# Kernel tuning notes

Hardware: AMD Instinct MI355X
Metric: run time of the kernel (lower is better)

Reference implementation:

```python
import jax, jax.numpy as jnp
import numpy as np

B, L, C, H = 2, 2048, 1024, 16  # batches, tokens per batch, channels, heads


def _ln(x, eps=1e-6):
    # LayerNorm32: no affine, eps=1e-6, computed in fp32
    x32 = x.astype(jnp.float32)
    m = x32.mean(-1, keepdims=True)
    v = ((x32 - m) ** 2).mean(-1, keepdims=True)
    return ((x32 - m) * jax.lax.rsqrt(v + eps)).astype(x.dtype)


def setup_inputs() -> dict:
    key = jax.random.key(0)
    ks = jax.random.split(key, 8)
    s = 0.02
    return {
        "feats": jax.random.normal(ks[0], (B * L, C), jnp.float32),
        "mod": jax.random.normal(ks[1], (B, C), jnp.float32),
        "w_mod": jax.random.normal(ks[2], (C, 6 * C), jnp.float32) * s,
        "b_mod": jnp.zeros((6 * C,), jnp.float32),
        "w_qkv": jax.random.normal(ks[3], (C, 3 * C), jnp.float32) * s,
        "b_qkv": jnp.zeros((3 * C,), jnp.float32),
        "w_proj": jax.random.normal(ks[4], (C, C), jnp.float32) * s,
        "b_proj": jnp.zeros((C,), jnp.float32),
        "w_fc1": jax.random.normal(ks[5], (C, 4 * C), jnp.float32) * s,
        "b_fc1": jnp.zeros((4 * C,), jnp.float32),
        "w_fc2": jax.random.normal(ks[6], (4 * C, C), jnp.float32) * s,
        "b_fc2": jnp.zeros((C,), jnp.float32),
        "seq_len": L,
    }


def reference(feats, mod, w_mod, b_mod, w_qkv, b_qkv, w_proj, b_proj,
              w_fc1, b_fc1, w_fc2, b_fc2, seq_len):
    Bn, Cn = mod.shape
    Ln = seq_len
    Hn = H
    D = Cn // Hn

    # adaLN modulation: SiLU -> Linear(C, 6C), chunk into 6 [B, C] pieces
    m = jax.nn.silu(mod) @ w_mod + b_mod
    sh_a, sc_a, g_a, sh_m, sc_m, g_m = jnp.split(m, 6, axis=1)

    x = feats.reshape(Bn, Ln, Cn)

    # --- MSA branch ---
    h = _ln(x)
    h = h * (1.0 + sc_a[:, None]) + sh_a[:, None]
    qkv = h @ w_qkv + b_qkv  # [B, L, 3C]
    q, k, v = [t.reshape(Bn, Ln, Hn, D) for t in jnp.split(qkv, 3, axis=-1)]
    scores = jnp.einsum('bqhd,bkhd->bhqk', q, k) / jnp.sqrt(jnp.float32(D))
    a = jax.nn.softmax(scores, axis=-1)
    o = jnp.einsum('bhqk,bkhd->bqhd', a, v).reshape(Bn, Ln, Cn)
    o = o @ w_proj + b_proj
    x = x + o * g_a[:, None]

    # --- FFN branch ---
    h = _ln(x)
    h = h * (1.0 + sc_m[:, None]) + sh_m[:, None]
    h = jax.nn.gelu(h @ w_fc1 + b_fc1, approximate=False) @ w_fc2 + b_fc2
    x = x + h * g_m[:, None]

    return x.reshape(Bn * Ln, Cn)
```

## Files before the change

### kernel.cpp

```cpp
#include <hip/hip_runtime.h>
#include <hip/hip_bf16.h>
#include <math.h>

#define B_ 2
#define L_ 2048
#define C_ 1024
#define H_ 16
#define D_ 64

typedef __attribute__((ext_vector_type(8))) short short8;
typedef __attribute__((ext_vector_type(4))) float float4v;

__device__ inline short f2bs(float f) {
    union { __hip_bfloat16 h; short s; } u; u.h = __float2bfloat16(f); return u.s;
}

#define GL2LDS(gp, lp)                                                         \
    __builtin_amdgcn_global_load_lds(                                          \
        (const __attribute__((address_space(1))) void*)(gp),                   \
        (__attribute__((address_space(3))) void*)(lp), 16, 0, 0)

__global__ __launch_bounds__(256) void k_mod2(const float* __restrict__ mod,
                                              const float* __restrict__ w_mod,
                                              const float* __restrict__ b_mod,
                                              float* __restrict__ m_out) {
    __shared__ float a_s[2][256];
    const int t = threadIdx.x;
    const int seg = blockIdx.y;
    for (int i = t; i < 512; i += 256) {
        float a = mod[(i >> 8) * C_ + seg * 256 + (i & 255)];
        a_s[i >> 8][i & 255] = a / (1.f + __expf(-a));
    }
    __syncthreads();
    int j = blockIdx.x * 256 + t;
    float acc0 = (seg == 0) ? b_mod[j] : 0.f;
    float acc1 = acc0;
    for (int k = 0; k < 256; ++k) {
        float w = w_mod[(size_t)(seg * 256 + k) * (6 * C_) + j];
        acc0 += a_s[0][k] * w;
        acc1 += a_s[1][k] * w;
    }
    atomicAdd(&m_out[j], acc0);
    atomicAdd(&m_out[6 * C_ + j], acc1);
}

__global__ __launch_bounds__(256) void k_wt_all(
        const float* __restrict__ w_qkv, const float* __restrict__ w_proj,
        const float* __restrict__ w_fc1, const float* __restrict__ w_fc2,
        short* __restrict__ wqkvT, short* __restrict__ wprojT,
        short* __restrict__ wfc1T, short* __restrict__ wfc2T) {
    __shared__ short T[64][72];
    int id = blockIdx.x;
    const float* W; short* WT; int K, N;
    if (id < 768)       {             W = w_qkv;  WT = wqkvT;  K = C_;     N = 3 * C_; }
    else if (id < 1024) { id -= 768;  W = w_proj; WT = wprojT; K = C_;     N = C_;     }
    else if (id < 2048) { id -= 1024; W = w_fc1;  WT = wfc1T;  K = C_;     N = 4 * C_; }
    else                { id -= 2048; W = w_fc2;  WT = wfc2T;  K = 4 * C_; N = C_;     }
    const int nb = N >> 6;
    const int n0 = (id % nb) * 64, k0 = (id / nb) * 64;
    const int t = threadIdx.x;
    {
        int kr = t >> 2, nc = (t & 3) * 16;
        const float* src = W + (size_t)(k0 + kr) * N + n0 + nc;
#pragma unroll
        for (int j = 0; j < 16; ++j) T[kr][nc + j] = f2bs(src[j]);
    }
    __syncthreads();
    {
        int nr = t >> 2, kc = (t & 3) * 16;
        short8 o0, o1;
#pragma unroll
        for (int j = 0; j < 8; ++j) { o0[j] = T[kc + j][nr]; o1[j] = T[kc + 8 + j][nr]; }
        short* dst = WT + (size_t)(n0 + nr) * K + k0 + kc;
        *(short8*)dst = o0;
        *(short8*)(dst + 8) = o1;
    }
}

__global__ __launch_bounds__(256) void k_vt(const __hip_bfloat16* __restrict__ qkv,
                                            short* __restrict__ vt) {
    __shared__ short T[64][72];
    const int t = threadIdx.x;
    const int kt = blockIdx.x * 64;
    const int bh = blockIdx.y;
    const int h = bh & (H_ - 1), b = bh >> 4;
    const __hip_bfloat16* src = qkv + ((size_t)(b * L_ + kt)) * (3 * C_) + 2 * C_ + h * D_;
    {
        int kr = t >> 2, dg = (t & 3) * 16;
        const short8* s = (const short8*)(src + (size_t)kr * (3 * C_) + dg);
        *(short8*)&T[kr][dg] = s[0];
        *(short8*)&T[kr][dg + 8] = s[1];
    }
    __syncthreads();
    {
        int dr = t >> 2, kg = (t & 3) * 16;
        short8 o0, o1;
#pragma unroll
        for (int j = 0; j < 8; ++j) { o0[j] = T[kg + j][dr]; o1[j] = T[kg + 8 + j][dr]; }
        short* dst = vt + ((size_t)bh * D_ + dr) * L_ + kt + kg;
        *(short8*)dst = o0;
        *(short8*)(dst + 8) = o1;
    }
}

__global__ __launch_bounds__(256) void k_ln_mod(const float* __restrict__ x,
                                                const float* __restrict__ mvec,
                                                int off_sh, int off_sc,
                                                __hip_bfloat16* __restrict__ h_out) {
    int row = blockIdx.x;
    int b = row / L_;
    int t = threadIdx.x;
    float v[4];
    float s = 0.f, ss = 0.f;
#pragma unroll
    for (int i = 0; i < 4; ++i) {
        int c = t + i * 256;
        float val = x[(size_t)row * C_ + c];
        v[i] = val; s += val; ss += val * val;
    }
#pragma unroll
    for (int o = 32; o; o >>= 1) { s += __shfl_xor(s, o); ss += __shfl_xor(ss, o); }
    __shared__ float red[2][4];
    int wid = t >> 6, lane = t & 63;
    if (lane == 0) { red[0][wid] = s; red[1][wid] = ss; }
    __syncthreads();
    s  = red[0][0] + red[0][1] + red[0][2] + red[0][3];
    ss = red[1][0] + red[1][1] + red[1][2] + red[1][3];
    float mean = s * (1.f / C_);
    float var  = ss * (1.f / C_) - mean * mean;
    float rstd = rsqrtf(var + 1e-6f);
#pragma unroll
    for (int i = 0; i < 4; ++i) {
        int c = t + i * 256;
        float sc = mvec[b * (6 * C_) + off_sc + c];
        float sh = mvec[b * (6 * C_) + off_sh + c];
        float hn = (v[i] - mean) * rstd;
        h_out[(size_t)row * C_ + c] = __float2bfloat16(hn * (1.f + sc) + sh);
    }
}

__device__ inline void gemm_epilogue(float v, int m, int n, int N, int act, int emode,
                                     const float* __restrict__ gate,
                                     const float* __restrict__ resid_f,
                                     __hip_bfloat16* __restrict__ out_bf,
                                     float* __restrict__ out_f) {
    if (act == 1) v = 0.5f * v * (1.f + erff(v * 0.70710678118654752440f));
    if (emode == 2) {
        float g = gate[(m >> 11) * (6 * C_) + n];
        v = resid_f[(size_t)m * N + n] + v * g;
    }
    if (out_f) out_f[(size_t)m * N + n] = v;
    else       out_bf[(size_t)m * N + n] = __float2bfloat16(v);
}

template<int WM, int WN, int MI, int NI>
__global__ __launch_bounds__(256) void k_gemm_async(
        const __hip_bfloat16* __restrict__ A, int lda,
        const short* __restrict__ WT, int ldw,
        const float* __restrict__ bias,
        int M, int N, int K, int act, int emode,
        const float* __restrict__ gate,
        const float* __restrict__ resid_f,
        __hip_bfloat16* __restrict__ out_bf,
        float* __restrict__ out_f) {
    constexpr int BM = WM * MI * 16;
    constexpr int BN = WN * NI * 16;
    __shared__ __align__(16) short A_lds[BM * 64];
    __shared__ __align__(16) short B_lds[BN * 64];
    const int t = threadIdx.x;
    const int lane = t & 63;
    const int w = t >> 6;
    const int wm = w / WN, wn = w % WN;
    const int quad = lane >> 4, l16 = lane & 15;
    const int m0 = blockIdx.y * BM;
    const int n0 = blockIdx.x * BN;

    float4v acc[MI][NI] = {};

    for (int k0 = 0; k0 < K; k0 += 64) {
        __syncthreads();
#pragma unroll
        for (int rep = 0; rep < BM / 32; ++rep) {
            int p = rep * 256 + t;
            int row = p >> 3;
            int g = (p & 7) ^ (row & 7);
            const __hip_bfloat16* gp = A + (size_t)(m0 + row) * lda + k0 + g * 8;
            GL2LDS(gp, &A_lds[(rep * 256 + (t & ~63)) * 8]);
        }
#pragma unroll
        for (int rep = 0; rep < BN / 32; ++rep) {
            int p = rep * 256 + t;
            int row = p >> 3;
            int g = (p & 7) ^ (row & 7);
            const short* gp = WT + (size_t)(n0 + row) * ldw + k0 + g * 8;
            GL2LDS(gp, &B_lds[(rep * 256 + (t & ~63)) * 8]);
        }
        __syncthreads();
        short8 af[MI][2], bf[NI][2];
#pragma unroll
        for (int mi = 0; mi < MI; ++mi) {
            int r = wm * MI * 16 + mi * 16 + l16;
#pragma unroll
            for (int h = 0; h < 2; ++h)
                af[mi][h] = *(const short8*)(&A_lds[(r * 8 + ((h * 4 + quad) ^ (r & 7))) * 8]);
        }
#pragma unroll
        for (int ni = 0; ni < NI; ++ni) {
            int r = wn * NI * 16 + ni * 16 + l16;
#pragma unroll
            for (int h = 0; h < 2; ++h)
                bf[ni][h] = *(const short8*)(&B_lds[(r * 8 + ((h * 4 + quad) ^ (r & 7))) * 8]);
        }
#pragma unroll
        for (int h = 0; h < 2; ++h)
#pragma unroll
            for (int mi = 0; mi < MI; ++mi)
#pragma unroll
                for (int ni = 0; ni < NI; ++ni)
                    acc[mi][ni] = __builtin_amdgcn_mfma_f32_16x16x32_bf16(
                        af[mi][h], bf[ni][h], acc[mi][ni], 0, 0, 0);
    }

#pragma unroll
    for (int mi = 0; mi < MI; ++mi)
#pragma unroll
        for (int ni = 0; ni < NI; ++ni)
#pragma unroll
            for (int r = 0; r < 4; ++r) {
                int m = m0 + wm * MI * 16 + mi * 16 + quad * 4 + r;
                int n = n0 + wn * NI * 16 + ni * 16 + l16;
                float v = acc[mi][ni][r] + (bias ? bias[n] : 0.f);
                gemm_epilogue(v, m, n, N, act, emode, gate, resid_f, out_bf, out_f);
            }
}

__global__ __launch_bounds__(512) void k_attn(const __hip_bfloat16* __restrict__ qkv,
                                              const short* __restrict__ vt,
                                              __hip_bfloat16* __restrict__ o) {
    __shared__ __align__(16) short K_lds[2][64 * 72];
    __shared__ __align__(16) short V_lds[2][64 * 72];
    __shared__ __align__(16) short P_lds[8][16 * 72];
    const int t = threadIdx.x;
    const int lane = t & 63;
    const int w = t >> 6;
    const int quad = lane >> 4, l16 = lane & 15;

    const int raw = blockIdx.x;
    const int blk = (raw & 7) * 64 + (raw >> 3);
    const int bh = blk >> 4;
    const int q_blk = (blk & 15) * 128;
    const int h = bh & (H_ - 1);
    const int b = bh >> 4;

    const size_t stride = 3 * C_;
    const __hip_bfloat16* base = qkv + (size_t)b * L_ * stride + h * D_;

    short8 qf[2];
    {
        const __hip_bfloat16* qrow = base + (size_t)(q_blk + w * 16 + l16) * stride;
        qf[0] = *(const short8*)(qrow + quad * 8);
        qf[1] = *(const short8*)(qrow + 32 + quad * 8);
    }
    short8 ones;
#pragma unroll
    for (int j = 0; j < 8; ++j) ones[j] = (short)0x3F80;

    float4v o_acc[4];
    float4v l_acc = (float4v){0.f, 0.f, 0.f, 0.f};
#pragma unroll
    for (int dt = 0; dt < 4; ++dt) o_acc[dt] = (float4v){0.f, 0.f, 0.f, 0.f};

    const int s_row = t >> 3;
    const int s_col = (t & 7) * 8;
    const __hip_bfloat16* kg = base + C_;
    const short* vtb = vt + (size_t)bh * D_ * L_;

    short8 kreg = *(const short8*)(kg + (size_t)s_row * stride + s_col);
    short8 vreg = *(const short8*)(vtb + (size_t)s_row * L_ + s_col);
    *(short8*)&K_lds[0][s_row * 72 + s_col] = kreg;
    *(short8*)&V_lds[0][s_row * 72 + s_col] = vreg;
    __syncthreads();

    for (int kt = 0, cur = 0; kt < L_; kt += 64, cur ^= 1) {
        const int nxt = kt + 64;
        if (nxt < L_) {
            kreg = *(const short8*)(kg + (size_t)(nxt + s_row) * stride + s_col);
            vreg = *(const short8*)(vtb + (size_t)s_row * L_ + nxt + s_col);
        }

        float4v sacc[4];
        __builtin_amdgcn_s_setprio(1);
#pragma unroll
        for (int kb = 0; kb < 4; ++kb) {
            sacc[kb] = (float4v){0.f, 0.f, 0.f, 0.f};
            short8 kf0 = *(const short8*)(&K_lds[cur][(kb * 16 + l16) * 72 + quad * 8]);
            short8 kf1 = *(const short8*)(&K_lds[cur][(kb * 16 + l16) * 72 + 32 + quad * 8]);
            sacc[kb] = __builtin_amdgcn_mfma_f32_16x16x32_bf16(qf[0], kf0, sacc[kb], 0, 0, 0);
            sacc[kb] = __builtin_amdgcn_mfma_f32_16x16x32_bf16(qf[1], kf1, sacc[kb], 0, 0, 0);
        }
        __builtin_amdgcn_s_setprio(0);

#pragma unroll
        for (int r = 0; r < 4; ++r) {
            short* prow = &P_lds[w][(quad * 4 + r) * 72];
            prow[l16]      = f2bs(__expf(fmaf(sacc[0][r], 0.125f, -8.f)));
            prow[16 + l16] = f2bs(__expf(fmaf(sacc[1][r], 0.125f, -8.f)));
            prow[32 + l16] = f2bs(__expf(fmaf(sacc[2][r], 0.125f, -8.f)));
            prow[48 + l16] = f2bs(__expf(fmaf(sacc[3][r], 0.125f, -8.f)));
        }

        short8 pf0 = *(const short8*)(&P_lds[w][l16 * 72 + quad * 8]);
        short8 pf1 = *(const short8*)(&P_lds[w][l16 * 72 + 32 + quad * 8]);
        __builtin_amdgcn_s_setprio(1);
        l_acc = __builtin_amdgcn_mfma_f32_16x16x32_bf16(pf0, ones, l_acc, 0, 0, 0);
        l_acc = __builtin_amdgcn_mfma_f32_16x16x32_bf16(pf1, ones, l_acc, 0, 0, 0);
#pragma unroll
        for (int dt = 0; dt < 4; ++dt) {
            short8 vf0 = *(const short8*)(&V_lds[cur][(dt * 16 + l16) * 72 + quad * 8]);
            short8 vf1 = *(const short8*)(&V_lds[cur][(dt * 16 + l16) * 72 + 32 + quad * 8]);
            o_acc[dt] = __builtin_amdgcn_mfma_f32_16x16x32_bf16(pf0, vf0, o_acc[dt], 0, 0, 0);
            o_acc[dt] = __builtin_amdgcn_mfma_f32_16x16x32_bf16(pf1, vf1, o_acc[dt], 0, 0, 0);
        }
        __builtin_amdgcn_s_setprio(0);

        if (nxt < L_) {
            *(short8*)&K_lds[cur ^ 1][s_row * 72 + s_col] = kreg;
            *(short8*)&V_lds[cur ^ 1][s_row * 72 + s_col] = vreg;
        }
        __syncthreads();
    }

#pragma unroll
    for (int dt = 0; dt < 4; ++dt)
#pragma unroll
        for (int r = 0; r < 4; ++r) {
            int q = q_blk + w * 16 + quad * 4 + r;
            o[(size_t)(b * L_ + q) * C_ + h * D_ + dt * 16 + l16] =
                __float2bfloat16(o_acc[dt][r] / l_acc[r]);
        }
}

extern "C" void kernel_launch(void* const* d_in, const int* in_sizes, int n_in,
                              void* d_out, int out_size, void* d_ws, size_t ws_size,
                              hipStream_t stream) {
    const float* feats  = (const float*)d_in[0];
    const float* mod    = (const float*)d_in[1];
    const float* w_mod  = (const float*)d_in[2];
    const float* b_mod  = (const float*)d_in[3];
    const float* w_qkv  = (const float*)d_in[4];
    const float* b_qkv  = (const float*)d_in[5];
    const float* w_proj = (const float*)d_in[6];
    const float* b_proj = (const float*)d_in[7];
    const float* w_fc1  = (const float*)d_in[8];
    const float* b_fc1  = (const float*)d_in[9];
    const float* w_fc2  = (const float*)d_in[10];
    const float* b_fc2  = (const float*)d_in[11];

    const int M = B_ * L_;
    char* ws = (char*)d_ws;
    float* m_ws = (float*)ws;

    short* wqkvT  = (short*)(ws + 49152);
    short* wprojT = wqkvT + (size_t)3 * C_ * C_;
    short* wfc1T  = wprojT + (size_t)C_ * C_;
    short* wfc2T  = wfc1T + (size_t)4 * C_ * C_;
    char* slotB = (char*)(wfc2T + (size_t)4 * C_ * C_);
    __hip_bfloat16* qkv_ws = (__hip_bfloat16*)slotB;
    float* x1_ws           = (float*)slotB;
    __hip_bfloat16* slotA  = (__hip_bfloat16*)(slotB + (size_t)M * 3 * C_ * 2);
    __hip_bfloat16* hf_ws  = slotA + (size_t)M * C_;
    short* vt_ws           = (short*)hf_ws;

    k_wt_all<<<3072, 256, 0, stream>>>(w_qkv, w_proj, w_fc1, w_fc2,
                                       wqkvT, wprojT, wfc1T, wfc2T);
    hipMemsetAsync(m_ws, 0, 2 * 6 * C_ * sizeof(float), stream);
    k_mod2<<<dim3(24, 4), 256, 0, stream>>>(mod, w_mod, b_mod, m_ws);
    k_ln_mod<<<M, 256, 0, stream>>>(feats, m_ws, 0, 1024, slotA);
    k_gemm_async<2, 2, 4, 4><<<dim3(3 * C_ / 128, M / 128), 256, 0, stream>>>(
        slotA, C_, wqkvT, C_, b_qkv, M, 3 * C_, C_, 0, 0,
        nullptr, nullptr, qkv_ws, nullptr);
    k_vt<<<dim3(L_ / 64, B_ * H_), 256, 0, stream>>>(qkv_ws, vt_ws);
    k_attn<<<B_ * H_ * (L_ / 128), 512, 0, stream>>>(qkv_ws, vt_ws, slotA);
    k_gemm_async<4, 1, 2, 4><<<dim3(C_ / 64, M / 128), 256, 0, stream>>>(
        slotA, C_, wprojT, C_, b_proj, M, C_, C_, 0, 2,
        m_ws + 2 * C_, feats, nullptr, x1_ws);
    k_ln_mod<<<M, 256, 0, stream>>>(x1_ws, m_ws, 3 * C_, 4 * C_, slotA);
    k_gemm_async<2, 2, 4, 4><<<dim3(4 * C_ / 128, M / 128), 256, 0, stream>>>(
        slotA, C_, wfc1T, C_, b_fc1, M, 4 * C_, C_, 1, 0,
        nullptr, nullptr, hf_ws, nullptr);
    k_gemm_async<4, 1, 2, 4><<<dim3(C_ / 64, M / 128), 256, 0, stream>>>(
        hf_ws, 4 * C_, wfc2T, 4 * C_, b_fc2, M, C_, 4 * C_, 0, 2,
        m_ws + 5 * C_, x1_ws, nullptr, (float*)d_out);
}
```

Baseline: 490.1 us.

## Double-buffer LDS tiles in async GEMM to overlap loads with MFMA

The bf16 MFMA GEMM kernel gets two LDS buffers for the A and B tiles. It issues the global-to-LDS async loads for the next K tile before computing on the current one, and needs only one barrier per iteration instead of two. The goal is to hide global memory latency behind the matrix-core work. In exchange, LDS use per block doubles, which may lower occupancy.

```diff
diff --git a/kernel.cpp b/kernel.cpp
--- a/kernel.cpp
+++ b/kernel.cpp
@@ -165,8 +165,8 @@
         float* __restrict__ out_f) {
     constexpr int BM = WM * MI * 16;
     constexpr int BN = WN * NI * 16;
-    __shared__ __align__(16) short A_lds[BM * 64];
-    __shared__ __align__(16) short B_lds[BN * 64];
+    __shared__ __align__(16) short A_lds[2][BM * 64];
+    __shared__ __align__(16) short B_lds[2][BN * 64];
     const int t = threadIdx.x;
     const int lane = t & 63;
     const int w = t >> 6;
@@ -175,17 +175,14 @@
     const int m0 = blockIdx.y * BM;
     const int n0 = blockIdx.x * BN;
 
-    float4v acc[MI][NI] = {};
-
-    for (int k0 = 0; k0 < K; k0 += 64) {
-        __syncthreads();
+    auto stage = [&](int buf, int k0) {
 #pragma unroll
         for (int rep = 0; rep < BM / 32; ++rep) {
             int p = rep * 256 + t;
             int row = p >> 3;
             int g = (p & 7) ^ (row & 7);
             const __hip_bfloat16* gp = A + (size_t)(m0 + row) * lda + k0 + g * 8;
-            GL2LDS(gp, &A_lds[(rep * 256 + (t & ~63)) * 8]);
+            GL2LDS(gp, &A_lds[buf][(rep * 256 + (t & ~63)) * 8]);
         }
 #pragma unroll
         for (int rep = 0; rep < BN / 32; ++rep) {
@@ -193,32 +190,46 @@
             int row = p >> 3;
             int g = (p & 7) ^ (row & 7);
             const short* gp = WT + (size_t)(n0 + row) * ldw + k0 + g * 8;
-            GL2LDS(gp, &B_lds[(rep * 256 + (t & ~63)) * 8]);
-        }
-        __syncthreads();
-        short8 af[MI][2], bf[NI][2];
+            GL2LDS(gp, &B_lds[buf][(rep * 256 + (t & ~63)) * 8]);
+        }
+    };
+
+    float4v acc[MI][NI] = {};
+
+    stage(0, 0);
+    __syncthreads();
+
+    const int nt = K >> 6;
+    int cur = 0;
+    for (int kt = 0; kt < nt; ++kt) {
+        if (kt + 1 < nt) stage(cur ^ 1, (kt + 1) << 6);
+
+        short8 af[MI][2], bfr[NI][2];
 #pragma unroll
         for (int mi = 0; mi < MI; ++mi) {
             int r = wm * MI * 16 + mi * 16 + l16;
 #pragma unroll
-            for (int h = 0; h < 2; ++h)
-                af[mi][h] = *(const short8*)(&A_lds[(r * 8 + ((h * 4 + quad) ^ (r & 7))) * 8]);
+            for (int hh = 0; hh < 2; ++hh)
+                af[mi][hh] = *(const short8*)(&A_lds[cur][(r * 8 + ((hh * 4 + quad) ^ (r & 7))) * 8]);
         }
 #pragma unroll
         for (int ni = 0; ni < NI; ++ni) {
             int r = wn * NI * 16 + ni * 16 + l16;
 #pragma unroll
-            for (int h = 0; h < 2; ++h)
-                bf[ni][h] = *(const short8*)(&B_lds[(r * 8 + ((h * 4 + quad) ^ (r & 7))) * 8]);
-        }
-#pragma unroll
-        for (int h = 0; h < 2; ++h)
+            for (int hh = 0; hh < 2; ++hh)
+                bfr[ni][hh] = *(const short8*)(&B_lds[cur][(r * 8 + ((hh * 4 + quad) ^ (r & 7))) * 8]);
+        }
+#pragma unroll
+        for (int hh = 0; hh < 2; ++hh)
 #pragma unroll
             for (int mi = 0; mi < MI; ++mi)
 #pragma unroll
                 for (int ni = 0; ni < NI; ++ni)
                     acc[mi][ni] = __builtin_amdgcn_mfma_f32_16x16x32_bf16(
-                        af[mi][h], bf[ni][h], acc[mi][ni], 0, 0, 0);
+                        af[mi][hh], bfr[ni][hh], acc[mi][ni], 0, 0, 0);
+
+        __syncthreads();
+        cur ^= 1;
     }
 
 #pragma unroll
```

Result: no change. 489.0 us (-0.2%).
